# Performance work log

Hardware: AMD Instinct MI355X
Metric: run time of the kernel (lower is better)

Reference implementation:

```python
import jax, jax.numpy as jnp
from jax import lax
import numpy as np
import math

N = 8
IN_CH = 3
EPS = 1e-6


def _dct_basis(n=N):
    # basis[u, i] = c(u) * cos(pi * u * (i + 0.5) / n)
    u = np.arange(n)
    i = np.arange(n)
    b = np.cos(np.pi * np.outer(u, i + 0.5) / n)
    c = np.full(n, math.sqrt(2.0 / n))
    c[0] = math.sqrt(1.0 / n)
    return b * c[:, None]


def _dct_conv_weight(n=N, in_ch=IN_CH):
    # weight[k = u*n + v, i, j] = basis[u,i] * basis[v,j]; grouped conv OIHW with I=1
    b = _dct_basis(n)
    w = np.einsum('ui,vj->uvij', b, b).reshape(n * n, 1, n, n).astype(np.float32)
    return np.concatenate([w] * in_ch, axis=0)  # [in_ch*n*n, 1, n, n]


def setup_inputs() -> dict:
    key = jax.random.key(0)
    k1, k2, k3 = jax.random.split(key, 3)
    B, C, H, W = 32, 3, 512, 512
    x = jax.random.uniform(k1, (B, C, H, W), dtype=jnp.float32)  # RGB in [0,1)
    # per-(sample, channel) stats; keep divisor d = max - min + eps > 1 so the
    # B-times repeated in-place normalization of the original stays finite
    max_ = 1.5 + jax.random.uniform(k2, (B, C * N * N, 1, 1), dtype=jnp.float32)
    min_ = 0.1 * jax.random.uniform(k3, (B, C * N * N, 1, 1), dtype=jnp.float32)
    ycbcr_w = jnp.asarray(
        [[0.299, 0.587, 0.114],
         [-0.169, -0.331, 0.5],
         [0.5, -0.419, -0.081]], dtype=jnp.float32)  # [out_c, in_c]
    dct_w = jnp.asarray(_dct_conv_weight())  # [192, 1, 8, 8]
    return {"x": x, "max_": max_, "min_": min_, "ycbcr_w": ycbcr_w, "dct_w": dct_w}


def reference(x, max_, min_, ycbcr_w, dct_w):
    # 1x1 RGB -> YCbCr conv == channel matmul
    ycbcr = jnp.einsum('oc,bchw->bohw', ycbcr_w, x)
    # grouped 8x8 stride-8 block-DCT conv: [B, 192, H/8, W/8]
    dct = lax.conv_general_dilated(
        ycbcr, dct_w, window_strides=(N, N), padding='VALID',
        feature_group_count=IN_CH,
        dimension_numbers=('NCHW', 'OIHW', 'NCHW'))
    # Original applies t = (t - min) / (max - min + eps) in-place B times per
    # sample (outer loop index i is unused but repeats the whole inner loop).
    d = max_ - min_ + EPS
    B = x.shape[0]
    out = lax.fori_loop(0, B, lambda i, t: (t - min_) / d, dct)
    return out
```

## Files before the change

kernel.cpp:

```cpp
#include <hip/hip_runtime.h>


#define HW 512
#define CHST (HW * HW)
#define NPAIR 6144
#define EPS 1e-6f

static constexpr float BASIS[8][8] = {
  { 0.35355339059327373f, 0.35355339059327373f, 0.35355339059327373f, 0.35355339059327373f,
    0.35355339059327373f, 0.35355339059327373f, 0.35355339059327373f, 0.35355339059327373f },
  { 0.49039264020161522f, 0.41573480615127262f, 0.27778511650980114f, 0.09754516100806412f,
   -0.09754516100806412f,-0.27778511650980114f,-0.41573480615127262f,-0.49039264020161522f },
  { 0.46193976625564337f, 0.19134171618254492f,-0.19134171618254492f,-0.46193976625564337f,
   -0.46193976625564337f,-0.19134171618254492f, 0.19134171618254492f, 0.46193976625564337f },
  { 0.41573480615127262f,-0.09754516100806412f,-0.49039264020161522f,-0.27778511650980114f,
    0.27778511650980114f, 0.49039264020161522f, 0.09754516100806412f,-0.41573480615127262f },
  { 0.35355339059327373f,-0.35355339059327373f,-0.35355339059327373f, 0.35355339059327373f,
    0.35355339059327373f,-0.35355339059327373f,-0.35355339059327373f, 0.35355339059327373f },
  { 0.27778511650980114f,-0.49039264020161522f, 0.09754516100806412f, 0.41573480615127262f,
   -0.41573480615127262f,-0.09754516100806412f, 0.49039264020161522f,-0.27778511650980114f },
  { 0.19134171618254492f,-0.46193976625564337f, 0.46193976625564337f,-0.19134171618254492f,
   -0.19134171618254492f, 0.46193976625564337f,-0.46193976625564337f, 0.19134171618254492f },
  { 0.09754516100806412f,-0.27778511650980114f, 0.41573480615127262f,-0.49039264020161522f,
    0.49039264020161522f,-0.41573480615127262f, 0.27778511650980114f,-0.09754516100806412f }
};

__global__ void precomp_norm(const float* __restrict__ max_,
                             const float* __restrict__ min_,
                             float* __restrict__ so) {
    int i = blockIdx.x * 256 + threadIdx.x;
    if (i >= NPAIR) return;
    float mn = min_[i], mx = max_[i];
    float d = mx - mn + EPS;
    float a = 1.0f / d;
    float a2 = a * a, a4 = a2 * a2, a8 = a4 * a4, a16 = a8 * a8, a32 = a16 * a16;
    float geo = a * (1.0f - a32) / (1.0f - a);
    so[2 * i]     = a32;
    so[2 * i + 1] = -mn * geo;
}

template <bool USE_WS>
__global__ __launch_bounds__(256, 3)
void dct_kernel(const float* __restrict__ x,
                const float* __restrict__ ycbcr_w,
                const float* __restrict__ so,
                const float* __restrict__ max_,
                const float* __restrict__ min_,
                float* __restrict__ out) {
    const int wt   = blockIdx.x * 4 + (threadIdx.x >> 6);
    const int lane = threadIdx.x & 63;
    const int rh   = lane >> 5;
    const int lx   = lane & 31;

    const int band = wt / 6;
    const int rem  = wt - band * 6;
    const int half = (rem >= 3) ? 1 : 0;
    const int c    = rem - half * 3;
    const int by   = band & 63;
    const int b    = band >> 6;
    const int bx   = half * 32 + lx;

    const float wr = ycbcr_w[3 * c];
    const float wg = ycbcr_w[3 * c + 1];
    const float wb = ycbcr_w[3 * c + 2];

    const float* base = x + (size_t)(b * 3) * CHST
                          + (size_t)(by * 8 + rh * 4) * HW + bx * 8;

    float4 Rv[4][2], Gv[4][2], Bv[4][2];
#pragma unroll
    for (int t = 0; t < 4; ++t) {
        const float* rp = base + t * HW;
        Rv[t][0] = *(const float4*)(rp);
        Rv[t][1] = *(const float4*)(rp + 4);
        Gv[t][0] = *(const float4*)(rp + CHST);
        Gv[t][1] = *(const float4*)(rp + CHST + 4);
        Bv[t][0] = *(const float4*)(rp + 2 * CHST);
        Bv[t][1] = *(const float4*)(rp + 2 * CHST + 4);
    }

    float acc[4][8];
#pragma unroll
    for (int u0 = 0; u0 < 4; ++u0)
#pragma unroll
        for (int v = 0; v < 8; ++v) acc[u0][v] = 0.0f;

#pragma unroll
    for (int t = 0; t < 4; ++t) {
        float y[8];
        y[0] = fmaf(wr, Rv[t][0].x, fmaf(wg, Gv[t][0].x, wb * Bv[t][0].x));
        y[1] = fmaf(wr, Rv[t][0].y, fmaf(wg, Gv[t][0].y, wb * Bv[t][0].y));
        y[2] = fmaf(wr, Rv[t][0].z, fmaf(wg, Gv[t][0].z, wb * Bv[t][0].z));
        y[3] = fmaf(wr, Rv[t][0].w, fmaf(wg, Gv[t][0].w, wb * Bv[t][0].w));
        y[4] = fmaf(wr, Rv[t][1].x, fmaf(wg, Gv[t][1].x, wb * Bv[t][1].x));
        y[5] = fmaf(wr, Rv[t][1].y, fmaf(wg, Gv[t][1].y, wb * Bv[t][1].y));
        y[6] = fmaf(wr, Rv[t][1].z, fmaf(wg, Gv[t][1].z, wb * Bv[t][1].z));
        y[7] = fmaf(wr, Rv[t][1].w, fmaf(wg, Gv[t][1].w, wb * Bv[t][1].w));

        float z[8];
#pragma unroll
        for (int v = 0; v < 8; ++v) {
            float zz = y[0] * BASIS[v][0];
#pragma unroll
            for (int j = 1; j < 8; ++j)
                zz = fmaf(y[j], BASIS[v][j], zz);
            z[v] = zz;
        }

        float pz[8];
#pragma unroll
        for (int v = 0; v < 8; ++v)
            pz[v] = __shfl_xor(z[v], 32, 64);

#pragma unroll
        for (int u0 = 0; u0 < 4; ++u0) {
            const float bo = rh ? BASIS[4 + u0][4 + t] : BASIS[u0][t];
            const float bp = rh ? BASIS[4 + u0][t]     : BASIS[u0][4 + t];
#pragma unroll
            for (int v = 0; v < 8; ++v)
                acc[u0][v] = fmaf(bo, z[v], fmaf(bp, pz[v], acc[u0][v]));
        }
    }

    const int obase = b * 192 + c * 64;
    const int uh    = rh * 4;
    float* op = out + ((size_t)obase * 64 + by) * 64 + bx;
    const float2* sop = (const float2*)so + obase;

#pragma unroll
    for (int u0 = 0; u0 < 4; ++u0) {
#pragma unroll
        for (int v = 0; v < 8; ++v) {
            const int k = (uh + u0) * 8 + v;
            float s, o;
            if (USE_WS) {
                float2 p = sop[k];
                s = p.x;
                o = p.y;
            } else {
                float mn = min_[obase + k], mx = max_[obase + k];
                float d  = mx - mn + EPS;
                float a  = 1.0f / d;
                float a2 = a * a, a4 = a2 * a2, a8 = a4 * a4, a16 = a8 * a8, a32 = a16 * a16;
                s = a32;
                o = -mn * (a * (1.0f - a32) / (1.0f - a));
            }
            op[(size_t)k * 4096] = fmaf(s, acc[u0][v], o);
        }
    }
}

extern "C" void kernel_launch(void* const* d_in, const int* in_sizes, int n_in,
                              void* d_out, int out_size, void* d_ws, size_t ws_size,
                              hipStream_t stream) {
    const float* x    = (const float*)d_in[0];
    const float* max_ = (const float*)d_in[1];
    const float* min_ = (const float*)d_in[2];
    const float* yw   = (const float*)d_in[3];
    float* out = (float*)d_out;
    float* so  = (float*)d_ws;

    const bool use_ws = (ws_size >= (size_t)NPAIR * 2 * sizeof(float));
    if (use_ws) {
        precomp_norm<<<(NPAIR + 255) / 256, 256, 0, stream>>>(max_, min_, so);
        dct_kernel<true><<<3072, 256, 0, stream>>>(x, yw, so, max_, min_, out);
    } else {
        dct_kernel<false><<<3072, 256, 0, stream>>>(x, yw, nullptr, max_, min_, out);
    }
}
```

Baseline: 191.4 us.

## Compute all three YCbCr channels per thread to reuse loaded RGB pixels

Each wave now loads the RGB block once and computes the DCT for all three output channels, instead of one wave per channel each reloading the same RGB data. This aims to cut global input reads threefold. It triples the accumulator registers per thread and reduces the number of waves, which may lower occupancy and latency hiding.

```diff
diff --git a/kernel.cpp b/kernel.cpp
--- a/kernel.cpp
+++ b/kernel.cpp
@@ -40,112 +40,113 @@
 }
 
 template <bool USE_WS>
-__global__ __launch_bounds__(256, 3)
+__global__ __launch_bounds__(128, 3)
 void dct_kernel(const float* __restrict__ x,
                 const float* __restrict__ ycbcr_w,
                 const float* __restrict__ so,
                 const float* __restrict__ max_,
                 const float* __restrict__ min_,
                 float* __restrict__ out) {
-    const int wt   = blockIdx.x * 4 + (threadIdx.x >> 6);
+    const int band = blockIdx.x;
+    const int half = threadIdx.x >> 6;
     const int lane = threadIdx.x & 63;
     const int rh   = lane >> 5;
     const int lx   = lane & 31;
 
-    const int band = wt / 6;
-    const int rem  = wt - band * 6;
-    const int half = (rem >= 3) ? 1 : 0;
-    const int c    = rem - half * 3;
     const int by   = band & 63;
     const int b    = band >> 6;
     const int bx   = half * 32 + lx;
 
-    const float wr = ycbcr_w[3 * c];
-    const float wg = ycbcr_w[3 * c + 1];
-    const float wb = ycbcr_w[3 * c + 2];
+    float w[9];
+#pragma unroll
+    for (int i = 0; i < 9; ++i) w[i] = ycbcr_w[i];
 
     const float* base = x + (size_t)(b * 3) * CHST
                           + (size_t)(by * 8 + rh * 4) * HW + bx * 8;
 
-    float4 Rv[4][2], Gv[4][2], Bv[4][2];
+    float acc[3][4][8];
+#pragma unroll
+    for (int c = 0; c < 3; ++c)
+#pragma unroll
+        for (int u0 = 0; u0 < 4; ++u0)
+#pragma unroll
+            for (int v = 0; v < 8; ++v) acc[c][u0][v] = 0.0f;
+
 #pragma unroll
     for (int t = 0; t < 4; ++t) {
         const float* rp = base + t * HW;
-        Rv[t][0] = *(const float4*)(rp);
-        Rv[t][1] = *(const float4*)(rp + 4);
-        Gv[t][0] = *(const float4*)(rp + CHST);
-        Gv[t][1] = *(const float4*)(rp + CHST + 4);
-        Bv[t][0] = *(const float4*)(rp + 2 * CHST);
-        Bv[t][1] = *(const float4*)(rp + 2 * CHST + 4);
+        float4 Ra = *(const float4*)(rp);
+        float4 Rb = *(const float4*)(rp + 4);
+        float4 Ga = *(const float4*)(rp + CHST);
+        float4 Gb = *(const float4*)(rp + CHST + 4);
+        float4 Ba = *(const float4*)(rp + 2 * CHST);
+        float4 Bb = *(const float4*)(rp + 2 * CHST + 4);
+
+        float R[8] = {Ra.x, Ra.y, Ra.z, Ra.w, Rb.x, Rb.y, Rb.z, Rb.w};
+        float G[8] = {Ga.x, Ga.y, Ga.z, Ga.w, Gb.x, Gb.y, Gb.z, Gb.w};
+        float B[8] = {Ba.x, Ba.y, Ba.z, Ba.w, Bb.x, Bb.y, Bb.z, Bb.w};
+
+#pragma unroll
+        for (int c = 0; c < 3; ++c) {
+            const float wr = w[3 * c], wg = w[3 * c + 1], wb = w[3 * c + 2];
+            float y[8];
+#pragma unroll
+            for (int j = 0; j < 8; ++j)
+                y[j] = fmaf(wr, R[j], fmaf(wg, G[j], wb * B[j]));
+
+            float z[8];
+#pragma unroll
+            for (int v = 0; v < 8; ++v) {
+                float zz = y[0] * BASIS[v][0];
+#pragma unroll
+                for (int j = 1; j < 8; ++j)
+                    zz = fmaf(y[j], BASIS[v][j], zz);
+                z[v] = zz;
+            }
+
+            float pz[8];
+#pragma unroll
+            for (int v = 0; v < 8; ++v)
+                pz[v] = __shfl_xor(z[v], 32, 64);
+
+#pragma unroll
+            for (int u0 = 0; u0 < 4; ++u0) {
+                const float bo = rh ? BASIS[4 + u0][4 + t] : BASIS[u0][t];
+                const float bp = rh ? BASIS[4 + u0][t]     : BASIS[u0][4 + t];
+#pragma unroll
+                for (int v = 0; v < 8; ++v)
+                    acc[c][u0][v] = fmaf(bo, z[v], fmaf(bp, pz[v], acc[c][u0][v]));
+            }
+        }
     }
 
-    float acc[4][8];
+    const int uh = rh * 4;
 #pragma unroll
-    for (int u0 = 0; u0 < 4; ++u0)
-#pragma unroll
-        for (int v = 0; v < 8; ++v) acc[u0][v] = 0.0f;
-
-#pragma unroll
-    for (int t = 0; t < 4; ++t) {
-        float y[8];
-        y[0] = fmaf(wr, Rv[t][0].x, fmaf(wg, Gv[t][0].x, wb * Bv[t][0].x));
-        y[1] = fmaf(wr, Rv[t][0].y, fmaf(wg, Gv[t][0].y, wb * Bv[t][0].y));
-        y[2] = fmaf(wr, Rv[t][0].z, fmaf(wg, Gv[t][0].z, wb * Bv[t][0].z));
-        y[3] = fmaf(wr, Rv[t][0].w, fmaf(wg, Gv[t][0].w, wb * Bv[t][0].w));
-        y[4] = fmaf(wr, Rv[t][1].x, fmaf(wg, Gv[t][1].x, wb * Bv[t][1].x));
-        y[5] = fmaf(wr, Rv[t][1].y, fmaf(wg, Gv[t][1].y, wb * Bv[t][1].y));
-        y[6] = fmaf(wr, Rv[t][1].z, fmaf(wg, Gv[t][1].z, wb * Bv[t][1].z));
-        y[7] = fmaf(wr, Rv[t][1].w, fmaf(wg, Gv[t][1].w, wb * Bv[t][1].w));
-
-        float z[8];
-#pragma unroll
-        for (int v = 0; v < 8; ++v) {
-            float zz = y[0] * BASIS[v][0];
-#pragma unroll
-            for (int j = 1; j < 8; ++j)
-                zz = fmaf(y[j], BASIS[v][j], zz);
-            z[v] = zz;
-        }
-
-        float pz[8];
-#pragma unroll
-        for (int v = 0; v < 8; ++v)
-            pz[v] = __shfl_xor(z[v], 32, 64);
+    for (int c = 0; c < 3; ++c) {
+        const int obase = b * 192 + c * 64;
+        float* op = out + ((size_t)obase * 64 + by) * 64 + bx;
+        const float2* sop = (const float2*)so + obase;
 
 #pragma unroll
         for (int u0 = 0; u0 < 4; ++u0) {
-            const float bo = rh ? BASIS[4 + u0][4 + t] : BASIS[u0][t];
-            const float bp = rh ? BASIS[4 + u0][t]     : BASIS[u0][4 + t];
 #pragma unroll
-            for (int v = 0; v < 8; ++v)
-                acc[u0][v] = fmaf(bo, z[v], fmaf(bp, pz[v], acc[u0][v]));
-        }
-    }
-
-    const int obase = b * 192 + c * 64;
-    const int uh    = rh * 4;
-    float* op = out + ((size_t)obase * 64 + by) * 64 + bx;
-    const float2* sop = (const float2*)so + obase;
-
-#pragma unroll
-    for (int u0 = 0; u0 < 4; ++u0) {
-#pragma unroll
-        for (int v = 0; v < 8; ++v) {
-            const int k = (uh + u0) * 8 + v;
-            float s, o;
-            if (USE_WS) {
-                float2 p = sop[k];
-                s = p.x;
-                o = p.y;
-            } else {
-                float mn = min_[obase + k], mx = max_[obase + k];
-                float d  = mx - mn + EPS;
-                float a  = 1.0f / d;
-                float a2 = a * a, a4 = a2 * a2, a8 = a4 * a4, a16 = a8 * a8, a32 = a16 * a16;
-                s = a32;
-                o = -mn * (a * (1.0f - a32) / (1.0f - a));
+            for (int v = 0; v < 8; ++v) {
+                const int k = (uh + u0) * 8 + v;
+                float s, o;
+                if (USE_WS) {
+                    float2 p = sop[k];
+                    s = p.x;
+                    o = p.y;
+                } else {
+                    float mn = min_[obase + k], mx = max_[obase + k];
+                    float d  = mx - mn + EPS;
+                    float a  = 1.0f / d;
+                    float a2 = a * a, a4 = a2 * a2, a8 = a4 * a4, a16 = a8 * a8, a32 = a16 * a16;
+                    s = a32;
+                    o = -mn * (a * (1.0f - a32) / (1.0f - a));
+                }
+                op[(size_t)k * 4096] = fmaf(s, acc[c][u0][v], o);
             }
-            op[(size_t)k * 4096] = fmaf(s, acc[u0][v], o);
         }
     }
 }
@@ -163,8 +164,8 @@
     const bool use_ws = (ws_size >= (size_t)NPAIR * 2 * sizeof(float));
     if (use_ws) {
         precomp_norm<<<(NPAIR + 255) / 256, 256, 0, stream>>>(max_, min_, so);
-        dct_kernel<true><<<3072, 256, 0, stream>>>(x, yw, so, max_, min_, out);
+        dct_kernel<true><<<2048, 128, 0, stream>>>(x, yw, so, max_, min_, out);
     } else {
-        dct_kernel<false><<<3072, 256, 0, stream>>>(x, yw, nullptr, max_, min_, out);
+        dct_kernel<false><<<2048, 128, 0, stream>>>(x, yw, nullptr, max_, min_, out);
     }
 }
```

Result: slower. 202.1 us (+5.6%).
